# Optimization experiments

Measured on AMD Instinct MI355X. Metric: run time of the kernel, lower is better.

The kernel has to match this reference:

```python
import jax, jax.numpy as jnp
import numpy as np

N_NODES = 100000
N_EDGES = 1600000
D_FEAT = 128
HIDDEN = 128
HEADS = 4
OUT_C = HIDDEN // HEADS  # 32
N_CLASSES = 10
N_GRAPHS = 64
NEG_SLOPE = 0.2


def glorot(key, shape, fan_in, fan_out):
    s = jnp.sqrt(6.0 / (fan_in + fan_out))
    return jax.random.uniform(key, shape, minval=-s, maxval=s, dtype=jnp.float32)


def setup_inputs() -> dict:
    key = jax.random.key(0)
    ks = jax.random.split(key, 24)
    x = jax.random.normal(ks[0], (N_NODES, D_FEAT), dtype=jnp.float32)
    src = jax.random.randint(ks[1], (N_EDGES,), 0, N_NODES, dtype=jnp.int32)
    off = jax.random.randint(ks[2], (N_EDGES,), 1, N_NODES, dtype=jnp.int32)
    dst = ((src + off) % N_NODES).astype(jnp.int32)  # guarantees no self-loops
    edge_index = jnp.stack([src, dst], axis=0)
    batch = jnp.sort(jax.random.randint(ks[3], (N_NODES,), 0, N_GRAPHS, dtype=jnp.int32))
    inp = {"x": x, "edge_index": edge_index, "batch": batch}
    # GATConv layer params: W [in, H*C] (lin_l == lin_r), att_l/att_r [H, C], bias [H*C]
    ins = [D_FEAT, HIDDEN, HIDDEN]
    for i in range(3):
        k = 4 + 4 * i
        inp[f"W{i+1}"] = glorot(ks[k], (ins[i], HEADS * OUT_C), ins[i], HEADS * OUT_C)
        inp[f"al{i+1}"] = glorot(ks[k + 1], (HEADS, OUT_C), HEADS * OUT_C, 1)
        inp[f"ar{i+1}"] = glorot(ks[k + 2], (HEADS, OUT_C), HEADS * OUT_C, 1)
        inp[f"b{i+1}"] = jnp.zeros((HEADS * OUT_C,), jnp.float32)
    inp["lin1_w"] = glorot(ks[16], (HIDDEN, HIDDEN), HIDDEN, HIDDEN)
    inp["lin1_b"] = jnp.zeros((HIDDEN,), jnp.float32)
    inp["lin2_w"] = glorot(ks[17], (HIDDEN, N_CLASSES), HIDDEN, N_CLASSES)
    inp["lin2_b"] = jnp.zeros((N_CLASSES,), jnp.float32)
    return inp


def gat_layer(x, src, dst, W, att_l, att_r, bias):
    n = x.shape[0]
    H, C = att_l.shape
    xw = (x @ W).reshape(n, H, C)                       # Theta x
    al = jnp.einsum('nhc,hc->nh', xw, att_l)
    ar = jnp.einsum('nhc,hc->nh', xw, att_r)
    loop = jnp.arange(n, dtype=src.dtype)
    s = jnp.concatenate([src, loop])                    # add self-loops
    d = jnp.concatenate([dst, loop])
    logits = jax.nn.leaky_relu(al[s] + ar[d], NEG_SLOPE)  # [E+N, H]
    m = jax.ops.segment_max(logits, d, num_segments=n)    # segment softmax over dst
    e = jnp.exp(logits - m[d])
    z = jax.ops.segment_sum(e, d, num_segments=n)
    alpha = e / z[d]
    msg = xw[s] * alpha[:, :, None]                     # [E+N, H, C]
    out = jax.ops.segment_sum(msg, d, num_segments=n)   # scatter-add aggregate
    return out.reshape(n, H * C) + bias


def reference(x, edge_index, batch,
              W1, al1, ar1, b1, W2, al2, ar2, b2, W3, al3, ar3, b3,
              lin1_w, lin1_b, lin2_w, lin2_b):
    src, dst = edge_index[0], edge_index[1]
    h = jax.nn.relu(gat_layer(x, src, dst, W1, al1, ar1, b1))
    h = jax.nn.relu(gat_layer(h, src, dst, W2, al2, ar2, b2))
    h = jax.nn.relu(gat_layer(h, src, dst, W3, al3, ar3, b3))
    last = h
    # global mean pool over graphs in the batch
    s = jax.ops.segment_sum(h, batch, num_segments=N_GRAPHS)
    cnt = jax.ops.segment_sum(jnp.ones((h.shape[0],), h.dtype), batch, num_segments=N_GRAPHS)
    pooled = s / jnp.maximum(cnt, 1.0)[:, None]
    g = jax.nn.relu(pooled @ lin1_w + lin1_b)           # dropout inactive (eval)
    logits = g @ lin2_w + lin2_b
    return (jax.nn.log_softmax(logits, axis=-1), last)
```

## Files before the change

kernel.cpp:

```cpp
#include <hip/hip_runtime.h>
#include <math.h>


#define LRELU(x) ((x) > 0.f ? (x) : 0.2f*(x))
#define SH 8
#define TILE 4096
#define EPT 16

typedef __attribute__((ext_vector_type(8))) short s16x8;
typedef __attribute__((ext_vector_type(4))) float f32x4;

__device__ inline unsigned short f2bf(float f){
  unsigned u = __float_as_uint(f);
  u += 0x7fff + ((u >> 16) & 1);
  return (unsigned short)(u >> 16);
}

__global__ void k_init(int* __restrict__ bcnt, float* __restrict__ psum){
  int t = threadIdx.x;
  bcnt[t] = 0; bcnt[256 + t] = 0;
  for (int i = t; i < 8192; i += 256) psum[i] = 0.f;
}

template<bool BF16IN>
__device__ __forceinline__ void gemm_body(
    unsigned short* Wt, unsigned short* Xl,
    const void* __restrict__ Xv, const float* __restrict__ W,
    const float* __restrict__ attl, const float* __restrict__ attr,
    unsigned short* __restrict__ XW, float* __restrict__ AL, float* __restrict__ AR,
    int n, int bid, int gstride)
{
  int t = threadIdx.x;
  int lane = t & 63, w = t >> 6;
  int l15 = lane & 15, quad = lane >> 4;
  for (int i = 0; i < 64; i++){
    int e = i*256 + t;
    int k = e >> 7, nn = e & 127;
    Wt[nn*128 + ((((k>>3) ^ (nn&15))<<3) | (k&7))] = f2bf(W[e]);
  }
  int ntiles = (n + 63) >> 6;
  int r_ = t >> 2, seg = t & 3;
  for (int tile = bid; tile < ntiles; tile += gstride){
    int row0 = tile << 6;
    __syncthreads();
    {
      int grow = row0 + r_;
      unsigned short* dp = &Xl[r_*136 + seg*32];
      if (grow < n){
        if (BF16IN){
          const uint4* gp = (const uint4*)((const unsigned short*)Xv + (size_t)grow*128 + seg*32);
          #pragma unroll
          for (int i = 0; i < 4; i++) ((uint4*)dp)[i] = gp[i];
        } else {
          const float4* gp = (const float4*)((const float*)Xv + (size_t)grow*128 + seg*32);
          #pragma unroll
          for (int i = 0; i < 8; i++){
            float4 v = gp[i];
            ((unsigned*)dp)[i*2]   = (unsigned)f2bf(v.x) | ((unsigned)f2bf(v.y) << 16);
            ((unsigned*)dp)[i*2+1] = (unsigned)f2bf(v.z) | ((unsigned)f2bf(v.w) << 16);
          }
        }
      } else {
        #pragma unroll
        for (int i = 0; i < 4; i++) ((uint4*)dp)[i] = make_uint4(0,0,0,0);
      }
    }
    __syncthreads();
    f32x4 acc[4][2];
    #pragma unroll
    for (int rt = 0; rt < 4; rt++){ acc[rt][0] = (f32x4){0,0,0,0}; acc[rt][1] = (f32x4){0,0,0,0}; }
    #pragma unroll
    for (int ks = 0; ks < 4; ks++){
      s16x8 b0 = *(const s16x8*)&Wt[(w*32 + l15)*128      + (((ks*4+quad) ^ l15)<<3)];
      s16x8 b1 = *(const s16x8*)&Wt[(w*32 + 16 + l15)*128 + (((ks*4+quad) ^ l15)<<3)];
      #pragma unroll
      for (int rt = 0; rt < 4; rt++){
        s16x8 a = *(const s16x8*)&Xl[(rt*16 + l15)*136 + ks*32 + quad*8];
        acc[rt][0] = __builtin_amdgcn_mfma_f32_16x16x32_bf16(a, b0, acc[rt][0], 0, 0, 0);
        acc[rt][1] = __builtin_amdgcn_mfma_f32_16x16x32_bf16(a, b1, acc[rt][1], 0, 0, 0);
      }
    }
    __syncthreads();
    #pragma unroll
    for (int rt = 0; rt < 4; rt++)
      #pragma unroll
      for (int c2 = 0; c2 < 2; c2++)
        #pragma unroll
        for (int r = 0; r < 4; r++)
          Xl[(rt*16 + quad*4 + r)*136 + w*32 + c2*16 + l15] = f2bf(acc[rt][c2][r]);
    __syncthreads();
    {
      int grow = row0 + r_;
      if (grow < n){
        const unsigned short* sp = &Xl[r_*136 + seg*32];
        uint4 uu[4];
        #pragma unroll
        for (int i = 0; i < 4; i++) uu[i] = ((const uint4*)sp)[i];
        unsigned short* gx = XW + (size_t)grow*128 + seg*32;
        #pragma unroll
        for (int i = 0; i < 4; i++) ((uint4*)gx)[i] = uu[i];
        const unsigned* up = (const unsigned*)uu;
        const float4* alp = (const float4*)(attl + seg*32);
        const float4* arp = (const float4*)(attr + seg*32);
        float pl = 0.f, pr = 0.f;
        #pragma unroll
        for (int i = 0; i < 8; i++){
          unsigned ua = up[i*2], ub = up[i*2+1];
          float x0 = __uint_as_float(ua << 16);
          float x1 = __uint_as_float(ua & 0xffff0000u);
          float x2 = __uint_as_float(ub << 16);
          float x3 = __uint_as_float(ub & 0xffff0000u);
          float4 av = alp[i];
          float4 rv = arp[i];
          pl += x0*av.x + x1*av.y + x2*av.z + x3*av.w;
          pr += x0*rv.x + x1*rv.y + x2*rv.z + x3*rv.w;
        }
        AL[grow*4 + seg] = pl;
        AR[grow*4 + seg] = pr;
      }
    }
  }
}

template<bool BF16IN>
__global__ __launch_bounds__(256) void k_gemm(
    const void* __restrict__ Xv, const float* __restrict__ W,
    const float* __restrict__ attl, const float* __restrict__ attr,
    unsigned short* __restrict__ XW, float* __restrict__ AL, float* __restrict__ AR, int n)
{
  __shared__ unsigned short Wt[128*128];
  __shared__ unsigned short Xl[64*136];
  gemm_body<BF16IN>(Wt, Xl, Xv, W, attl, attr, XW, AL, AR, n, blockIdx.x, gridDim.x);
}

__global__ __launch_bounds__(256) void k_fuse1(
    const int* __restrict__ dst, int* __restrict__ bcnt, int E, int nparts,
    const float* __restrict__ X, const float* __restrict__ W,
    const float* __restrict__ attl, const float* __restrict__ attr,
    unsigned short* __restrict__ XW, float* __restrict__ AL, float* __restrict__ AR, int n)
{
  __shared__ unsigned short Wt[128*128];
  __shared__ unsigned short Xl[64*136];
  if ((int)blockIdx.x < nparts){
    int* lh = (int*)Wt;
    int t = threadIdx.x;
    for (int j = t; j < 512; j += 256) lh[j] = 0;
    __syncthreads();
    int base = blockIdx.x * TILE;
    int lim = min(base + TILE, E);
    for (int e = base + t; e < lim; e += 256)
      atomicAdd(&lh[dst[e] >> SH], 1);
    __syncthreads();
    for (int j = t; j < 512; j += 256){
      int v = lh[j];
      if (v) atomicAdd(&bcnt[j], v);
    }
    return;
  }
  gemm_body<false>(Wt, Xl, X, W, attl, attr, XW, AL, AR, n,
                   (int)blockIdx.x - nparts, (int)gridDim.x - nparts);
}

__global__ __launch_bounds__(256) void k_bscan(const int* __restrict__ bcnt,
    int* __restrict__ bstart, int* __restrict__ bfill, int NB, int E,
    const int* __restrict__ batch, int* __restrict__ gstart, int n){
  int t = threadIdx.x;
  if (blockIdx.x == 1){
    int g = t;
    if (g > 64) return;
    int lo = 0, hi = n;
    while (lo < hi){
      int mid = (lo + hi) >> 1;
      if (batch[mid] < g) lo = mid + 1; else hi = mid;
    }
    gstart[g] = lo;
    return;
  }
  __shared__ int c[512];
  __shared__ int ps[256];
  for (int j = t; j < 512; j += 256) c[j] = (j < NB) ? bcnt[j] : 0;
  __syncthreads();
  int b0 = 2*t;
  int v0 = c[b0], v1 = c[b0+1];
  int ts = v0 + v1;
  ps[t] = ts; __syncthreads();
  for (int off = 1; off < 256; off <<= 1){
    int x = (t >= off) ? ps[t-off] : 0; __syncthreads();
    ps[t] += x; __syncthreads();
  }
  int pre = ps[t] - ts;
  if (b0   < NB){ bstart[b0]   = pre;    bfill[b0]   = pre; }
  if (b0+1 < NB){ bstart[b0+1] = pre+v0; bfill[b0+1] = pre+v0; }
  if (t == 0) bstart[NB] = E;
}

__global__ __launch_bounds__(256) void k_part(const int* __restrict__ src,
    const int* __restrict__ dst, int* __restrict__ bfill,
    int2* __restrict__ tmp, int E){
  __shared__ int2 reorder[TILE];
  __shared__ int lhist[512], lscan[512], lgbase[512];
  __shared__ int ps[256];
  int t = threadIdx.x;
  int tb = blockIdx.x * TILE;
  int tilecnt = min(TILE, E - tb);
  for (int j = t; j < 512; j += 256) lhist[j] = 0;
  __syncthreads();
  int ss[EPT], dd[EPT], rk[EPT];
  #pragma unroll
  for (int i = 0; i < EPT; i++){
    int e = tb + t + i*256;
    if (e < E){
      ss[i] = src[e]; dd[i] = dst[e];
      rk[i] = atomicAdd(&lhist[dd[i] >> SH], 1);
    }
  }
  __syncthreads();
  int b0 = 2*t;
  int v0 = lhist[b0], v1 = lhist[b0+1];
  int ts = v0 + v1;
  ps[t] = ts; __syncthreads();
  for (int off = 1; off < 256; off <<= 1){
    int x = (t >= off) ? ps[t-off] : 0; __syncthreads();
    ps[t] += x; __syncthreads();
  }
  int pre = ps[t] - ts;
  int ex0 = pre, ex1 = pre + v0;
  lscan[b0] = ex0; lscan[b0+1] = ex1;
  if (v0 > 0){ int gb = atomicAdd(&bfill[b0],   v0); lgbase[b0]   = gb - ex0; }
  if (v1 > 0){ int gb = atomicAdd(&bfill[b0+1], v1); lgbase[b0+1] = gb - ex1; }
  __syncthreads();
  #pragma unroll
  for (int i = 0; i < EPT; i++){
    int e = tb + t + i*256;
    if (e < E){
      int b = dd[i] >> SH;
      reorder[lscan[b] + rk[i]] = make_int2(ss[i], dd[i]);
    }
  }
  __syncthreads();
  for (int j = t; j < tilecnt; j += 256){
    int2 p = reorder[j];
    tmp[lgbase[p.y >> SH] + j] = p;
  }
}

__global__ __launch_bounds__(256) void k_csr(const int2* __restrict__ tmp,
    const int* __restrict__ bstart, int* __restrict__ rp, int* __restrict__ col,
    int n, int E){
  __shared__ int lcnt[256];
  __shared__ int sc[256];
  int b = blockIdx.x, t = threadIdx.x;
  int node0 = b << SH;
  int ncnt = min(256, n - node0);
  int be = bstart[b], ee = bstart[b+1];
  lcnt[t] = 0;
  __syncthreads();
  for (int e = be + t; e < ee; e += 256)
    atomicAdd(&lcnt[tmp[e].y - node0], 1);
  __syncthreads();
  int v = lcnt[t];
  sc[t] = v;
  __syncthreads();
  for (int off = 1; off < 256; off <<= 1){
    int x = (t >= off) ? sc[t-off] : 0;
    __syncthreads();
    sc[t] += x;
    __syncthreads();
  }
  int start = be + sc[t] - v;
  lcnt[t] = start;
  if (t < ncnt) rp[node0 + t] = start;
  if (t == 0 && node0 + ncnt == n) rp[n] = E;
  __syncthreads();
  for (int e = be + t; e < ee; e += 256){
    int2 p = tmp[e];
    int pos = atomicAdd(&lcnt[p.y - node0], 1);
    col[pos] = p.x;
  }
}

template<bool BF16OUT>
__global__ __launch_bounds__(256) void k_attn(
    const unsigned short* __restrict__ XW, const float* __restrict__ AL, const float* __restrict__ AR,
    const int* __restrict__ rp, const int* __restrict__ col,
    const float* __restrict__ bias, void* __restrict__ OUT, int n)
{
  __shared__ float ebuf[4][64*4];
  __shared__ int   sbuf[4][64];
  int wv = threadIdx.x >> 6;
  int d = blockIdx.x*4 + wv;
  int lane = threadIdx.x & 63;
  if (d >= n) return;
  int start = rp[d], end = rp[d+1];
  float4 ald4 = ((const float4*)AL)[d];
  float4 ard4 = ((const float4*)AR)[d];
  float ar0 = ard4.x, ar1 = ard4.y, ar2 = ard4.z, ar3 = ard4.w;
  float es0 = __expf(LRELU(ald4.x + ar0));
  float es1 = __expf(LRELU(ald4.y + ar1));
  float es2 = __expf(LRELU(ald4.z + ar2));
  float es3 = __expf(LRELU(ald4.w + ar3));
  int h = lane >> 4;
  float eself = h==0?es0 : h==1?es1 : h==2?es2 : es3;
  const unsigned* XWr = (const unsigned*)XW;
  unsigned v = XWr[(unsigned)d*64 + lane];
  float acc0 = eself * __uint_as_float(v << 16);
  float acc1 = eself * __uint_as_float(v & 0xffff0000u);
  float zl0 = 0.f, zl1 = 0.f, zl2 = 0.f, zl3 = 0.f;
  float* eb = ebuf[wv];
  int*   sb = sbuf[wv];
  for (int base = start; base < end; base += 64){
    int cnt = min(64, end - base);
    int s = (lane < cnt) ? col[base + lane] : 0;
    float4 a = ((const float4*)AL)[s];
    float w0 = __expf(LRELU(a.x + ar0));
    float w1 = __expf(LRELU(a.y + ar1));
    float w2 = __expf(LRELU(a.z + ar2));
    float w3 = __expf(LRELU(a.w + ar3));
    if (lane >= cnt){ w0 = w1 = w2 = w3 = 0.f; }
    zl0 += w0; zl1 += w1; zl2 += w2; zl3 += w3;
    float4 w4; w4.x = w0; w4.y = w1; w4.z = w2; w4.w = w3;
    ((float4*)eb)[lane] = w4;
    sb[lane] = s << 6;
    #pragma unroll 8
    for (int j = 0; j < cnt; j++){
      unsigned sj = (unsigned)sb[j] + lane;
      float w = eb[j*4 + h];
      unsigned u = XWr[sj];
      acc0 = fmaf(w, __uint_as_float(u << 16), acc0);
      acc1 = fmaf(w, __uint_as_float(u & 0xffff0000u), acc1);
    }
  }
  #pragma unroll
  for (int off = 32; off >= 1; off >>= 1){
    zl0 += __shfl_xor(zl0, off, 64);
    zl1 += __shfl_xor(zl1, off, 64);
    zl2 += __shfl_xor(zl2, off, 64);
    zl3 += __shfl_xor(zl3, off, 64);
  }
  float z_h = (h==0?zl0 : h==1?zl1 : h==2?zl2 : zl3) + eself;
  float rz = 1.f / z_h;
  int ch = lane*2;
  float o0 = fmaf(acc0, rz, bias[ch]);
  float o1 = fmaf(acc1, rz, bias[ch+1]);
  o0 = o0 > 0.f ? o0 : 0.f;
  o1 = o1 > 0.f ? o1 : 0.f;
  if (BF16OUT){
    unsigned pk = (unsigned)f2bf(o0) | ((unsigned)f2bf(o1) << 16);
    ((unsigned*)OUT)[(unsigned)d*64 + lane] = pk;
  } else {
    float2 o; o.x = o0; o.y = o1;
    ((float2*)OUT)[(unsigned)d*64 + lane] = o;
  }
}

__global__ __launch_bounds__(128) void k_pool(const float* __restrict__ H,
                                              const int* __restrict__ gstart,
                                              float* __restrict__ psum){
  int g = blockIdx.x >> 3, slice = blockIdx.x & 7, t = threadIdx.x;
  int s0 = gstart[g], s1 = gstart[g+1];
  int cntg = s1 - s0;
  int chunk = (cntg + 7) >> 3;
  int lo = s0 + slice*chunk;
  int hi = min(lo + chunk, s1);
  float sum = 0.f;
  for (int i = lo; i < hi; i++) sum += H[(size_t)i*128 + t];
  atomicAdd(&psum[g*128 + t], sum);
}

__global__ __launch_bounds__(128) void k_mlp(const float* __restrict__ psum,
                       const int* __restrict__ gstart,
                       const float* __restrict__ w1, const float* __restrict__ b1,
                       const float* __restrict__ w2, const float* __restrict__ b2,
                       float* __restrict__ out)
{
  __shared__ float p[128];
  __shared__ float gsh[128];
  __shared__ float lg[10];
  int g = blockIdx.x, t = threadIdx.x;
  float c = fmaxf((float)(gstart[g+1] - gstart[g]), 1.f);
  p[t] = psum[g*128 + t] / c;
  __syncthreads();
  float acc = b1[t];
  for (int k = 0; k < 128; k++) acc = fmaf(p[k], w1[k*128 + t], acc);
  gsh[t] = acc > 0.f ? acc : 0.f;
  __syncthreads();
  if (t < 10){
    float a = b2[t];
    for (int k = 0; k < 128; k++) a = fmaf(gsh[k], w2[k*10 + t], a);
    lg[t] = a;
  }
  __syncthreads();
  if (t < 10){
    float mx = lg[0];
    for (int c2 = 1; c2 < 10; c2++) mx = fmaxf(mx, lg[c2]);
    float se = 0.f;
    for (int c2 = 0; c2 < 10; c2++) se += __expf(lg[c2] - mx);
    out[g*10 + t] = lg[t] - mx - logf(se);
  }
}

extern "C" void kernel_launch(void* const* d_in, const int* in_sizes, int n_in,
                              void* d_out, int out_size, void* d_ws, size_t ws_size,
                              hipStream_t stream)
{
  const float* x    = (const float*)d_in[0];
  const int* eidx   = (const int*)d_in[1];
  const int* batch  = (const int*)d_in[2];
  const float* W[3]  = {(const float*)d_in[3], (const float*)d_in[7],  (const float*)d_in[11]};
  const float* al[3] = {(const float*)d_in[4], (const float*)d_in[8],  (const float*)d_in[12]};
  const float* ar[3] = {(const float*)d_in[5], (const float*)d_in[9],  (const float*)d_in[13]};
  const float* bs[3] = {(const float*)d_in[6], (const float*)d_in[10], (const float*)d_in[14]};
  const float* l1w = (const float*)d_in[15];
  const float* l1b = (const float*)d_in[16];
  const float* l2w = (const float*)d_in[17];
  const float* l2b = (const float*)d_in[18];
  int E = in_sizes[1] / 2;
  int n = in_sizes[2];
  const int* srcp = eidx;
  const int* dstp = eidx + E;
  int NB = (n + 255) >> SH;

  char* wsp = (char*)d_ws;
  auto alloc = [&](size_t bytes){ void* p = (void*)wsp; wsp += (bytes + 255) & ~(size_t)255; return p; };
  unsigned short* xw   = (unsigned short*)alloc((size_t)n*128*2);
  unsigned short* hbuf = (unsigned short*)alloc((size_t)n*128*2);
  float* ALb  = (float*)alloc((size_t)n*4*4);
  float* ARb  = (float*)alloc((size_t)n*4*4);
  int* rp     = (int*)alloc((size_t)(n+1)*4);
  int* col    = (int*)alloc((size_t)E*4);
  int2* tmp   = (int2*)alloc((size_t)E*8);
  int* bcnt   = (int*)alloc(512*4);
  int* bstart = (int*)alloc(513*4);
  int* bfill  = (int*)alloc(512*4);
  float* psum = (float*)alloc(64*128*4);
  int* gstart = (int*)alloc(65*4);

  float* outlog = (float*)d_out;
  float* h3     = (float*)d_out + 64*10;

  int nparts = (E + TILE - 1) / TILE;

  k_init<<<1, 256, 0, stream>>>(bcnt, psum);
  k_fuse1<<<nparts + 768, 256, 0, stream>>>(dstp, bcnt, E, nparts,
                                            x, W[0], al[0], ar[0], xw, ALb, ARb, n);
  k_bscan<<<2, 256, 0, stream>>>(bcnt, bstart, bfill, NB, E, batch, gstart, n);
  k_part <<<nparts, 256, 0, stream>>>(srcp, dstp, bfill, tmp, E);
  k_csr  <<<NB, 256, 0, stream>>>(tmp, bstart, rp, col, n, E);

  k_attn<true><<<(n+3)/4, 256, 0, stream>>>(xw, ALb, ARb, rp, col, bs[0], hbuf, n);
  k_gemm<true><<<768, 256, 0, stream>>>(hbuf, W[1], al[1], ar[1], xw, ALb, ARb, n);
  k_attn<true><<<(n+3)/4, 256, 0, stream>>>(xw, ALb, ARb, rp, col, bs[1], hbuf, n);
  k_gemm<true><<<768, 256, 0, stream>>>(hbuf, W[2], al[2], ar[2], xw, ALb, ARb, n);
  k_attn<false><<<(n+3)/4, 256, 0, stream>>>(xw, ALb, ARb, rp, col, bs[2], h3, n);

  k_pool<<<64*8, 128, 0, stream>>>(h3, gstart, psum);
  k_mlp <<<64, 128, 0, stream>>>(psum, gstart, l1w, l1b, l2w, l2b, outlog);
}
```

Measured before the change: 579.5 us.

## Gather four neighbor rows per wave with 16-byte loads in GAT attention

Restructures the attention aggregation so each wave splits into four 16-lane groups, each loading a whole 256-byte bf16 row with uint4 loads, which handles four neighbors per inner iteration instead of one. Partial accumulators are reduced across groups with shuffles, and group 0 writes vectorized output. The aim is fewer, wider gather instructions and more memory parallelism per iteration. In exchange it needs padded shared buffers for tail neighbors, eight accumulators per lane and an extra cross-lane reduction.

```diff
diff --git a/kernel.cpp b/kernel.cpp
--- a/kernel.cpp
+++ b/kernel.cpp
@@ -285,12 +285,16 @@
     const int* __restrict__ rp, const int* __restrict__ col,
     const float* __restrict__ bias, void* __restrict__ OUT, int n)
 {
-  __shared__ float ebuf[4][64*4];
-  __shared__ int   sbuf[4][64];
+  __shared__ float ebuf[4][68*4];
+  __shared__ int   sbuf[4][68];
   int wv = threadIdx.x >> 6;
   int d = blockIdx.x*4 + wv;
   int lane = threadIdx.x & 63;
   if (d >= n) return;
+  float* eb = ebuf[wv];
+  int*   sb = sbuf[wv];
+  if (lane < 16) eb[256 + lane] = 0.f;
+  if (lane < 4)  sb[64 + lane] = 0;
   int start = rp[d], end = rp[d+1];
   float4 ald4 = ((const float4*)AL)[d];
   float4 ard4 = ((const float4*)AR)[d];
@@ -299,15 +303,25 @@
   float es1 = __expf(LRELU(ald4.y + ar1));
   float es2 = __expf(LRELU(ald4.z + ar2));
   float es3 = __expf(LRELU(ald4.w + ar3));
-  int h = lane >> 4;
-  float eself = h==0?es0 : h==1?es1 : h==2?es2 : es3;
-  const unsigned* XWr = (const unsigned*)XW;
-  unsigned v = XWr[(unsigned)d*64 + lane];
-  float acc0 = eself * __uint_as_float(v << 16);
-  float acc1 = eself * __uint_as_float(v & 0xffff0000u);
+  int r   = lane & 15;
+  int row = lane >> 4;
+  int h2  = r >> 2;
+  float eself = h2==0?es0 : h2==1?es1 : h2==2?es2 : es3;
+  const uint4* XW4 = (const uint4*)XW;
+  float acc[8];
+  {
+    uint4 v = XW4[(unsigned)d*16 + r];
+    float sw = (row == 0) ? eself : 0.f;
+    acc[0] = sw * __uint_as_float(v.x << 16);
+    acc[1] = sw * __uint_as_float(v.x & 0xffff0000u);
+    acc[2] = sw * __uint_as_float(v.y << 16);
+    acc[3] = sw * __uint_as_float(v.y & 0xffff0000u);
+    acc[4] = sw * __uint_as_float(v.z << 16);
+    acc[5] = sw * __uint_as_float(v.z & 0xffff0000u);
+    acc[6] = sw * __uint_as_float(v.w << 16);
+    acc[7] = sw * __uint_as_float(v.w & 0xffff0000u);
+  }
   float zl0 = 0.f, zl1 = 0.f, zl2 = 0.f, zl3 = 0.f;
-  float* eb = ebuf[wv];
-  int*   sb = sbuf[wv];
   for (int base = start; base < end; base += 64){
     int cnt = min(64, end - base);
     int s = (lane < cnt) ? col[base + lane] : 0;
@@ -320,14 +334,21 @@
     zl0 += w0; zl1 += w1; zl2 += w2; zl3 += w3;
     float4 w4; w4.x = w0; w4.y = w1; w4.z = w2; w4.w = w3;
     ((float4*)eb)[lane] = w4;
-    sb[lane] = s << 6;
-    #pragma unroll 8
-    for (int j = 0; j < cnt; j++){
-      unsigned sj = (unsigned)sb[j] + lane;
-      float w = eb[j*4 + h];
-      unsigned u = XWr[sj];
-      acc0 = fmaf(w, __uint_as_float(u << 16), acc0);
-      acc1 = fmaf(w, __uint_as_float(u & 0xffff0000u), acc1);
+    sb[lane] = s << 4;
+    #pragma unroll 4
+    for (int j = 0; j < cnt; j += 4){
+      int jr = j + row;
+      int sj = sb[jr] + r;
+      float w = eb[jr*4 + h2];
+      uint4 u = XW4[sj];
+      acc[0] = fmaf(w, __uint_as_float(u.x << 16), acc[0]);
+      acc[1] = fmaf(w, __uint_as_float(u.x & 0xffff0000u), acc[1]);
+      acc[2] = fmaf(w, __uint_as_float(u.y << 16), acc[2]);
+      acc[3] = fmaf(w, __uint_as_float(u.y & 0xffff0000u), acc[3]);
+      acc[4] = fmaf(w, __uint_as_float(u.z << 16), acc[4]);
+      acc[5] = fmaf(w, __uint_as_float(u.z & 0xffff0000u), acc[5]);
+      acc[6] = fmaf(w, __uint_as_float(u.w << 16), acc[6]);
+      acc[7] = fmaf(w, __uint_as_float(u.w & 0xffff0000u), acc[7]);
     }
   }
   #pragma unroll
@@ -337,19 +358,36 @@
     zl2 += __shfl_xor(zl2, off, 64);
     zl3 += __shfl_xor(zl3, off, 64);
   }
-  float z_h = (h==0?zl0 : h==1?zl1 : h==2?zl2 : zl3) + eself;
+  #pragma unroll
+  for (int i = 0; i < 8; i++){
+    acc[i] += __shfl_xor(acc[i], 16, 64);
+    acc[i] += __shfl_xor(acc[i], 32, 64);
+  }
+  float z_h = (h2==0?zl0 : h2==1?zl1 : h2==2?zl2 : zl3) + eself;
   float rz = 1.f / z_h;
-  int ch = lane*2;
-  float o0 = fmaf(acc0, rz, bias[ch]);
-  float o1 = fmaf(acc1, rz, bias[ch+1]);
-  o0 = o0 > 0.f ? o0 : 0.f;
-  o1 = o1 > 0.f ? o1 : 0.f;
-  if (BF16OUT){
-    unsigned pk = (unsigned)f2bf(o0) | ((unsigned)f2bf(o1) << 16);
-    ((unsigned*)OUT)[(unsigned)d*64 + lane] = pk;
-  } else {
-    float2 o; o.x = o0; o.y = o1;
-    ((float2*)OUT)[(unsigned)d*64 + lane] = o;
+  float4 b0 = ((const float4*)bias)[r*2];
+  float4 b1 = ((const float4*)bias)[r*2 + 1];
+  float o[8];
+  o[0] = fmaf(acc[0], rz, b0.x); o[1] = fmaf(acc[1], rz, b0.y);
+  o[2] = fmaf(acc[2], rz, b0.z); o[3] = fmaf(acc[3], rz, b0.w);
+  o[4] = fmaf(acc[4], rz, b1.x); o[5] = fmaf(acc[5], rz, b1.y);
+  o[6] = fmaf(acc[6], rz, b1.z); o[7] = fmaf(acc[7], rz, b1.w);
+  #pragma unroll
+  for (int i = 0; i < 8; i++) o[i] = o[i] > 0.f ? o[i] : 0.f;
+  if (row == 0){
+    if (BF16OUT){
+      uint4 pk;
+      pk.x = (unsigned)f2bf(o[0]) | ((unsigned)f2bf(o[1]) << 16);
+      pk.y = (unsigned)f2bf(o[2]) | ((unsigned)f2bf(o[3]) << 16);
+      pk.z = (unsigned)f2bf(o[4]) | ((unsigned)f2bf(o[5]) << 16);
+      pk.w = (unsigned)f2bf(o[6]) | ((unsigned)f2bf(o[7]) << 16);
+      ((uint4*)OUT)[(unsigned)d*16 + r] = pk;
+    } else {
+      float4 f0; f0.x = o[0]; f0.y = o[1]; f0.z = o[2]; f0.w = o[3];
+      float4 f1; f1.x = o[4]; f1.y = o[5]; f1.z = o[6]; f1.w = o[7];
+      ((float4*)OUT)[(unsigned)d*32 + r*2]     = f0;
+      ((float4*)OUT)[(unsigned)d*32 + r*2 + 1] = f1;
+    }
   }
 }
 
```

Result: slower. 593.1 us (+2.4%).
